# Kernel optimization log

Hardware: AMD Instinct MI355X
Metric: run time of the kernel (lower is better)

## Reference

```python
import jax, jax.numpy as jnp
import numpy as np

B, T, D, H, L = 2, 2048, 2048, 16, 64
HD = D // H  # 128
EPS = 1e-5


def setup_inputs() -> dict:
    key = jax.random.key(0)
    ks = jax.random.split(key, 16)
    s = 0.02
    inp = {
        'x': jax.random.normal(ks[0], (B, T, D), jnp.float32),
        'mask': jnp.tril(jnp.ones((T, T), dtype=bool)),
        'ln_w': jnp.ones((D,), jnp.float32),
        'ln_b': jnp.zeros((D,), jnp.float32),
        'wq': jax.random.normal(ks[1], (D, D), jnp.float32) * s,
        'bq': jnp.zeros((D,), jnp.float32),
        'wk': jax.random.normal(ks[2], (D, D), jnp.float32) * s,
        'bk': jnp.zeros((D,), jnp.float32),
        'wv': jax.random.normal(ks[3], (D, D), jnp.float32) * s,
        'bv': jnp.zeros((D,), jnp.float32),
        'wo': jax.random.normal(ks[4], (D, D), jnp.float32) * s,
        'bo': jnp.zeros((D,), jnp.float32),
        'wcq': jax.random.normal(ks[5], (HD, L), jnp.float32) * s,
        'bcq': jnp.zeros((L,), jnp.float32),
        'wck': jax.random.normal(ks[6], (HD, L), jnp.float32) * s,
        'bck': jnp.zeros((L,), jnp.float32),
        'wcv': jax.random.normal(ks[7], (HD, L), jnp.float32) * s,
        'bcv': jnp.zeros((L,), jnp.float32),
        'wd': jax.random.normal(ks[8], (L, HD), jnp.float32) * s,
        'bd': jnp.zeros((HD,), jnp.float32),
    }
    # standard RoPE frequency table: theta_i = 10000^{-2i/HD}
    inv_freq = 1.0 / (10000.0 ** (jnp.arange(0, HD, 2, dtype=jnp.float32) / HD))
    ang = jnp.arange(T, dtype=jnp.float32)[:, None] * inv_freq[None, :]  # [T, HD/2]
    inp['freqs_cos'] = jnp.cos(ang)
    inp['freqs_sin'] = jnp.sin(ang)
    return inp


def _rope(x, cos, sin):
    # x: [B,T,H,HD]; cos/sin: [T, HD/2]; interleaved (even=real, odd=imag)
    xr, xi = x[..., 0::2], x[..., 1::2]
    c = cos[None, :, None, :]
    sn = sin[None, :, None, :]
    out_r = xr * c - xi * sn
    out_i = xr * sn + xi * c
    return jnp.stack([out_r, out_i], axis=-1).reshape(x.shape)


def reference(x, mask, freqs_cos, freqs_sin, ln_w, ln_b, wq, bq, wk, bk, wv, bv,
              wo, bo, wcq, bcq, wck, bck, wcv, bcv, wd, bd):
    # LayerNorm
    mu = jnp.mean(x, axis=-1, keepdims=True)
    var = jnp.mean(jnp.square(x - mu), axis=-1, keepdims=True)
    xn = (x - mu) / jnp.sqrt(var + EPS) * ln_w + ln_b

    q = (xn @ wq + bq).reshape(B, T, H, HD)
    k = (xn @ wk + bk).reshape(B, T, H, HD)
    v = (xn @ wv + bv).reshape(B, T, H, HD)

    q, k = _rope(q, freqs_cos, freqs_sin), _rope(k, freqs_cos, freqs_sin)

    # compress each head to the latent dim
    q_lat = q @ wcq + bcq  # [B,T,H,L]
    k_lat = k @ wck + bck
    v_lat = v @ wcv + bcv

    scale = 1.0 / np.sqrt(L).astype(np.float32)
    scores = jnp.einsum('bqhl,bkhl->bhqk', q_lat, k_lat) * scale  # [B,H,T,T]
    additive = jnp.where(mask, 0.0, -1e9).astype(scores.dtype)  # bool mask -> additive
    scores = scores + additive[None, None, :, :]
    attn = jax.nn.softmax(scores, axis=-1)

    out = jnp.einsum('bhqk,bkhl->bqhl', attn, v_lat)  # [B,T,H,L]
    out = (out @ wd + bd).reshape(B, T, D)  # decompress to head_dim, merge heads
    return out @ wo + bo
```

## Files before the change

### kernel.cpp

```cpp
#include <hip/hip_runtime.h>
#include <hip/hip_bf16.h>
#include <stdint.h>

#define BB 2
#define TB 2048
#define DB 2048
#define HB 16
#define HDB 128
#define LB 64
#define MB 4096

typedef __hip_bfloat16 bf16;
typedef __attribute__((ext_vector_type(8))) short bf16x8;
typedef __attribute__((ext_vector_type(4))) float f32x4;

#define MFMA_16x16x32 __builtin_amdgcn_mfma_f32_16x16x32_bf16

typedef __attribute__((address_space(3))) void lds_t;
typedef const __attribute__((address_space(1))) void gvm_t;

static __device__ __forceinline__ float bf2f(bf16 h) { return __bfloat162float(h); }
static __device__ __forceinline__ bf16 f2bf(float f) { return __float2bfloat16(f); }
union BV8 { bf16x8 v; bf16 e[8]; };

#define SWZC(r) (((r) ^ ((r) >> 3)) & 7)

__device__ void do_ln(const float* __restrict__ x, const float* __restrict__ g,
                      const float* __restrict__ be, bf16* __restrict__ xn,
                      int row, int tid, char* sm) {
  float* red = (float*)sm;
  const float4* xr = (const float4*)(x + (size_t)row * DB);
  float4 a = xr[2 * tid], b = xr[2 * tid + 1];
  float s = a.x + a.y + a.z + a.w + b.x + b.y + b.z + b.w;
  float s2 = a.x * a.x + a.y * a.y + a.z * a.z + a.w * a.w +
             b.x * b.x + b.y * b.y + b.z * b.z + b.w * b.w;
  for (int off = 32; off > 0; off >>= 1) {
    s += __shfl_down(s, off);
    s2 += __shfl_down(s2, off);
  }
  int w = tid >> 6, lane = tid & 63;
  if (lane == 0) { red[w] = s; red[4 + w] = s2; }
  __syncthreads();
  s = red[0] + red[1] + red[2] + red[3];
  s2 = red[4] + red[5] + red[6] + red[7];
  float mu = s * (1.f / DB);
  float var = s2 * (1.f / DB) - mu * mu;
  float rstd = rsqrtf(var + 1e-5f);
  const float4* gw = (const float4*)g;
  const float4* bb = (const float4*)be;
  float4 g0 = gw[2 * tid], g1 = gw[2 * tid + 1];
  float4 b0 = bb[2 * tid], b1 = bb[2 * tid + 1];
  BV8 u;
  u.e[0] = f2bf((a.x - mu) * rstd * g0.x + b0.x);
  u.e[1] = f2bf((a.y - mu) * rstd * g0.y + b0.y);
  u.e[2] = f2bf((a.z - mu) * rstd * g0.z + b0.z);
  u.e[3] = f2bf((a.w - mu) * rstd * g0.w + b0.w);
  u.e[4] = f2bf((b.x - mu) * rstd * g1.x + b1.x);
  u.e[5] = f2bf((b.y - mu) * rstd * g1.y + b1.y);
  u.e[6] = f2bf((b.z - mu) * rstd * g1.z + b1.z);
  u.e[7] = f2bf((b.w - mu) * rstd * g1.w + b1.w);
  *(bf16x8*)(xn + (size_t)row * DB + tid * 8) = u.v;
}

__device__ void do_wconv(const float* __restrict__ W, bf16* __restrict__ Wt,
                         int bx, int by, int tid, char* sm) {
  float(*t)[33] = (float(*)[33])sm;
  int c0 = bx * 32, r0 = by * 32;
  int tx = tid & 31, ty = tid >> 5;
  for (int p = 0; p < 4; ++p)
    t[ty + 8 * p][tx] = W[(size_t)(r0 + ty + 8 * p) * DB + c0 + tx];
  __syncthreads();
  for (int p = 0; p < 4; ++p)
    Wt[(size_t)(c0 + ty + 8 * p) * DB + r0 + tx] = f2bf(t[tx][ty + 8 * p]);
}

__device__ void do_fold_v(const float* __restrict__ wv, const float* __restrict__ wcv,
                          bf16* __restrict__ BtV, int bx, int h, int tid, char* sm) {
  float(*wvs)[36] = (float(*)[36])sm;
  int k0 = bx * 128;
  int l = tid & 63, ks = tid >> 6;
  float acc[32];
#pragma unroll
  for (int i = 0; i < 32; ++i) acc[i] = 0.f;
  for (int dc = 0; dc < 128; dc += 32) {
    __syncthreads();
    for (int i = tid; i < 128 * 32; i += 256) {
      int kk = i >> 5, dd = i & 31;
      wvs[kk][dd] = wv[(size_t)(k0 + kk) * DB + h * 128 + dc + dd];
    }
    __syncthreads();
    float wr[32];
#pragma unroll
    for (int dd = 0; dd < 32; ++dd) wr[dd] = wcv[(dc + dd) * 64 + l];
#pragma unroll
    for (int i = 0; i < 32; ++i) {
      const float4* row = (const float4*)&wvs[ks * 32 + i][0];
#pragma unroll
      for (int d4 = 0; d4 < 8; ++d4) {
        float4 w4 = row[d4];
        acc[i] += w4.x * wr[d4 * 4] + w4.y * wr[d4 * 4 + 1] +
                  w4.z * wr[d4 * 4 + 2] + w4.w * wr[d4 * 4 + 3];
      }
    }
  }
  bf16* dst = BtV + (size_t)(h * 64 + l) * DB + k0 + ks * 32;
#pragma unroll
  for (int i8 = 0; i8 < 4; ++i8) {
    BV8 u;
#pragma unroll
    for (int j = 0; j < 8; ++j) u.e[j] = f2bf(acc[i8 * 8 + j]);
    *(bf16x8*)(dst + i8 * 8) = u.v;
  }
}

__device__ void do_fold_o(const float* __restrict__ wo, const float* __restrict__ wd,
                          bf16* __restrict__ BtO, int bx, int h, int tid, char* sm) {
  float(*wos)[132] = (float(*)[132])sm;
  int n0 = bx * 128;
  int l = tid & 63, ns = tid >> 6;
  float acc[32];
#pragma unroll
  for (int i = 0; i < 32; ++i) acc[i] = 0.f;
  for (int dc = 0; dc < 128; dc += 32) {
    __syncthreads();
    for (int i = tid; i < 32 * 128; i += 256) {
      int dd = i >> 7, nn = i & 127;
      wos[dd][nn] = wo[(size_t)(h * 128 + dc + dd) * DB + n0 + nn];
    }
    __syncthreads();
    float wr[32];
#pragma unroll
    for (int d4 = 0; d4 < 8; ++d4) {
      float4 w4 = *(const float4*)&wd[l * 128 + dc + d4 * 4];
      wr[d4 * 4] = w4.x; wr[d4 * 4 + 1] = w4.y;
      wr[d4 * 4 + 2] = w4.z; wr[d4 * 4 + 3] = w4.w;
    }
#pragma unroll
    for (int dd = 0; dd < 32; ++dd) {
      float w = wr[dd];
      const float4* row = (const float4*)&wos[dd][ns * 32];
#pragma unroll
      for (int i4 = 0; i4 < 8; ++i4) {
        float4 a4 = row[i4];
        acc[i4 * 4 + 0] += a4.x * w; acc[i4 * 4 + 1] += a4.y * w;
        acc[i4 * 4 + 2] += a4.z * w; acc[i4 * 4 + 3] += a4.w * w;
      }
    }
  }
#pragma unroll
  for (int i = 0; i < 32; ++i)
    BtO[(size_t)(n0 + ns * 32 + i) * 1024 + h * 64 + l] = f2bf(acc[i]);
}

__global__ __launch_bounds__(256) void prep_kernel(
    const float* __restrict__ x, const float* __restrict__ ln_w,
    const float* __restrict__ ln_b, bf16* __restrict__ xn,
    const float* __restrict__ wq, const float* __restrict__ wk,
    bf16* __restrict__ wqkT,
    const float* __restrict__ wv, const float* __restrict__ wcv,
    bf16* __restrict__ BtV,
    const float* __restrict__ wo, const float* __restrict__ wd,
    bf16* __restrict__ BtO,
    const float* __restrict__ bv, const float* __restrict__ bcv,
    float* __restrict__ bvlat,
    const float* __restrict__ bd, const float* __restrict__ bo,
    float* __restrict__ bo2) {
  __shared__ __align__(16) char sm[18432];
  int b = blockIdx.x, tid = threadIdx.x;
  if (b < 4096) {
    do_ln(x, ln_w, ln_b, xn, b, tid, sm);
  } else if (b < 8192) {
    int bb = b - 4096;
    do_wconv(wq, wqkT, bb & 63, bb >> 6, tid, sm);
  } else if (b < 12288) {
    int bb = b - 8192;
    do_wconv(wk, wqkT + (size_t)2048 * 2048, bb & 63, bb >> 6, tid, sm);
  } else if (b < 12544) {
    int bb = b - 12288;
    do_fold_v(wv, wcv, BtV, bb & 15, bb >> 4, tid, sm);
  } else if (b < 12800) {
    int bb = b - 12544;
    do_fold_o(wo, wd, BtO, bb & 15, bb >> 4, tid, sm);
  } else if (b < 12804) {
    int j = (b - 12800) * 256 + tid;
    int h = j >> 6, l = j & 63;
    float s = bcv[l];
    for (int d = 0; d < 128; ++d) s += bv[h * 128 + d] * wcv[d * 64 + l];
    bvlat[j] = s;
  } else {
    float(*red)[64] = (float(*)[64])sm;
    int nl = tid & 63, ks = tid >> 6;
    int n = (b - 12804) * 64 + nl;
    float s = 0.f;
    for (int k = ks * 512; k < ks * 512 + 512; ++k)
      s += bd[k & 127] * wo[(size_t)k * DB + n];
    red[ks][nl] = s;
    __syncthreads();
    if (ks == 0) bo2[n] = bo[n] + red[0][nl] + red[1][nl] + red[2][nl] + red[3][nl];
  }
}

__global__ __launch_bounds__(256) void gemm_qkv_kernel(
    const bf16* __restrict__ A, const bf16* __restrict__ wqkT,
    const bf16* __restrict__ BtV,
    const float* __restrict__ bq, const float* __restrict__ bk,
    const float* __restrict__ bvl,
    const float* __restrict__ wcq, const float* __restrict__ wck,
    const float* __restrict__ bcq, const float* __restrict__ bck,
    bf16* __restrict__ qlat, bf16* __restrict__ klat, bf16* __restrict__ vlatT,
    const float* __restrict__ fcos, const float* __restrict__ fsin) {
  constexpr int K = DB;
  __shared__ __align__(16) char smem[49152];
  bf16* As = (bf16*)smem;
  bf16* Bs = (bf16*)(smem + 8192);
  bf16* Qt = (bf16*)smem;
  bf16* Wt = (bf16*)(smem + 32768);
  int tid = threadIdx.x;
  int m0 = blockIdx.y * 128, n0 = blockIdx.x * 128;
  int w = tid >> 6, l = tid & 63;
  int wr = w >> 1, wc = w & 1;
  int lrow = l & 15, lk = (l >> 4) * 8, ck = l >> 4;
  const bf16* Bsrc = (n0 < 4096) ? (wqkT + (size_t)n0 * K)
                                 : (BtV + (size_t)(n0 - 4096) * K);
  int sel = n0 >> 11;

  if (sel < 2) {
    const float* wcp = sel == 0 ? wcq : wck;
    for (int i = tid; i < 8192; i += 256) {
      int d = i >> 6, j = i & 63;
      Wt[j * 128 + (((d >> 3) ^ (j & 7)) * 8) + (d & 7)] = f2bf(wcp[d * 64 + j]);
    }
  }

  f32x4 zero4 = {0.f, 0.f, 0.f, 0.f};
  f32x4 acc[4][4];
  for (int m = 0; m < 4; ++m)
    for (int n = 0; n < 4; ++n) acc[m][n] = zero4;

  for (int kk = 0; kk < K / 32; ++kk) {
    int k0 = kk * 32;
    __syncthreads();
#pragma unroll
    for (int i = 0; i < 2; ++i) {
      int c = i * 256 + tid;
      int r = c >> 2, cc = c & 3;
      int cb = i * 256 + (tid & ~63);
      __builtin_amdgcn_global_load_lds(
          (gvm_t*)&A[(size_t)(m0 + r) * K + k0 + cc * 8], (lds_t*)&As[cb * 8], 16, 0, 0);
      __builtin_amdgcn_global_load_lds(
          (gvm_t*)&Bsrc[(size_t)r * K + k0 + cc * 8], (lds_t*)&Bs[cb * 8], 16, 0, 0);
    }
    __syncthreads();
    bf16x8 af[4], bfr[4];
    for (int m = 0; m < 4; ++m)
      af[m] = *(bf16x8*)&As[(wr * 64 + m * 16 + lrow) * 32 + lk];
    for (int n = 0; n < 4; ++n)
      bfr[n] = *(bf16x8*)&Bs[(wc * 64 + n * 16 + lrow) * 32 + lk];
    for (int m = 0; m < 4; ++m)
      for (int n = 0; n < 4; ++n)
        acc[m][n] = MFMA_16x16x32(af[m], bfr[n], acc[m][n], 0, 0, 0);
  }

  int rg = 4 * (l >> 4), cl = l & 15;
  if (sel == 2) {
    for (int mf = 0; mf < 4; ++mf) {
      int rowb = m0 + wr * 64 + mf * 16 + rg;
      for (int nf = 0; nf < 4; ++nf) {
        int col = n0 + wc * 64 + nf * 16 + cl;
        int colV = col - 4096;
        float bv_ = bvl[colV];
        size_t vbase = ((size_t)((rowb >> 11) * HB + (colV >> 6)) * 64 + (colV & 63)) * TB
                       + (rowb & (TB - 1));
        for (int r = 0; r < 4; ++r)
          vlatT[vbase + r] = f2bf(acc[mf][nf][r] + bv_);
      }
    }
    return;
  }

  const float* bias = sel == 0 ? bq : bk;
  __syncthreads();
  for (int mf = 0; mf < 4; ++mf) {
    int rowb = m0 + wr * 64 + mf * 16 + rg;
    int rl0 = wr * 64 + mf * 16 + rg;
    for (int nf = 0; nf < 4; ++nf) {
      int col = n0 + wc * 64 + nf * 16 + cl;
      int colL = col & 2047;
      int cloc = wc * 64 + nf * 16 + cl;
      float bv_ = bias[colL];
      for (int r = 0; r < 4; ++r) {
        int rr = rowb + r;
        float v = acc[mf][nf][r] + bv_;
        float pv = __shfl_xor(v, 1);
        int t = rr & (TB - 1);
        int pi = (col & 127) >> 1;
        float c = fcos[t * 64 + pi], sn = fsin[t * 64 + pi];
        v = (col & 1) ? (pv * sn + v * c) : (v * c - pv * sn);
        int rl = rl0 + r;
        Qt[rl * 128 + ((((cloc >> 3) ^ (rl & 7)) * 8) + (cloc & 7))] = f2bf(v);
      }
    }
  }
  __syncthreads();
  f32x4 pacc[2][4];
#pragma unroll
  for (int mi = 0; mi < 2; ++mi)
#pragma unroll
    for (int nf = 0; nf < 4; ++nf) pacc[mi][nf] = zero4;
#pragma unroll
  for (int kc = 0; kc < 4; ++kc) {
    bf16x8 aq[2], bw[4];
#pragma unroll
    for (int mi = 0; mi < 2; ++mi) {
      int row = w * 32 + mi * 16 + lrow;
      aq[mi] = *(bf16x8*)&Qt[row * 128 + (((kc * 4 + ck) ^ (row & 7)) * 8)];
    }
#pragma unroll
    for (int nf = 0; nf < 4; ++nf) {
      int jrow = nf * 16 + lrow;
      bw[nf] = *(bf16x8*)&Wt[jrow * 128 + (((kc * 4 + ck) ^ (jrow & 7)) * 8)];
    }
#pragma unroll
    for (int mi = 0; mi < 2; ++mi)
#pragma unroll
      for (int nf = 0; nf < 4; ++nf)
        pacc[mi][nf] = MFMA_16x16x32(aq[mi], bw[nf], pacc[mi][nf], 0, 0, 0);
  }
  int head = (n0 & 2047) >> 7;
  const float* bias2 = sel == 0 ? bcq : bck;
  bf16* outp = sel == 0 ? qlat : klat;
#pragma unroll
  for (int mi = 0; mi < 2; ++mi)
#pragma unroll
    for (int nf = 0; nf < 4; ++nf) {
      int colj = nf * 16 + cl;
      float b2 = bias2[colj];
#pragma unroll
      for (int r = 0; r < 4; ++r) {
        int roG = m0 + w * 32 + mi * 16 + rg + r;
        outp[((size_t)roG * HB + head) * 64 + colj] = f2bf(pacc[mi][nf][r] + b2);
      }
    }
}

__global__ __launch_bounds__(256) void gemm_out_kernel(
    const bf16* __restrict__ A, const bf16* __restrict__ Bt,
    const float* __restrict__ bias, float* __restrict__ Cout) {
  constexpr int K = 1024, N = DB;
  __shared__ __align__(16) bf16 As[128 * 32];
  __shared__ __align__(16) bf16 Bs[128 * 32];
  int tid = threadIdx.x;
  int m0 = blockIdx.y * 128, n0 = blockIdx.x * 128;
  int w = tid >> 6, l = tid & 63;
  int wr = w >> 1, wc = w & 1;
  int lrow = l & 15, lk = (l >> 4) * 8;

  f32x4 zero4 = {0.f, 0.f, 0.f, 0.f};
  f32x4 acc[4][4];
  for (int m = 0; m < 4; ++m)
    for (int n = 0; n < 4; ++n) acc[m][n] = zero4;

  for (int kk = 0; kk < K / 32; ++kk) {
    int k0 = kk * 32;
    __syncthreads();
#pragma unroll
    for (int i = 0; i < 2; ++i) {
      int c = i * 256 + tid;
      int r = c >> 2, cc = c & 3;
      int cb = i * 256 + (tid & ~63);
      __builtin_amdgcn_global_load_lds(
          (gvm_t*)&A[(size_t)(m0 + r) * K + k0 + cc * 8], (lds_t*)&As[cb * 8], 16, 0, 0);
      __builtin_amdgcn_global_load_lds(
          (gvm_t*)&Bt[(size_t)(n0 + r) * K + k0 + cc * 8], (lds_t*)&Bs[cb * 8], 16, 0, 0);
    }
    __syncthreads();
    bf16x8 af[4], bfr[4];
    for (int m = 0; m < 4; ++m)
      af[m] = *(bf16x8*)&As[(wr * 64 + m * 16 + lrow) * 32 + lk];
    for (int n = 0; n < 4; ++n)
      bfr[n] = *(bf16x8*)&Bs[(wc * 64 + n * 16 + lrow) * 32 + lk];
    for (int m = 0; m < 4; ++m)
      for (int n = 0; n < 4; ++n)
        acc[m][n] = MFMA_16x16x32(af[m], bfr[n], acc[m][n], 0, 0, 0);
  }

  int rg = 4 * (l >> 4), cl = l & 15;
  for (int m = 0; m < 4; ++m) {
    int rowb = m0 + wr * 64 + m * 16 + rg;
    for (int n = 0; n < 4; ++n) {
      int col = n0 + wc * 64 + n * 16 + cl;
      float bv = bias[col];
      for (int r = 0; r < 4; ++r)
        Cout[(size_t)(rowb + r) * N + col] = acc[m][n][r] + bv;
    }
  }
}

__global__ __launch_bounds__(256) void attn_kernel(const bf16* __restrict__ qlat,
                                                   const bf16* __restrict__ klat,
                                                   const bf16* __restrict__ vlatT,
                                                   bf16* __restrict__ aout) {
  int tid = threadIdx.x, w = tid >> 6, l = tid & 63;
  int job = ((int)blockIdx.x & 7) * 64 + ((int)blockIdx.x >> 3);
  int bh = job >> 4, pair = job & 15;
  int h = bh & 15, b = bh >> 4;
  int lrow = l & 15, ck = l >> 4, hi4 = l >> 4;
  __shared__ __align__(16) bf16 Ks[64 * 64];
  __shared__ __align__(16) bf16 VsT[64 * 64];
  __shared__ __align__(16) bf16 Ps[4][16 * 64];
  f32x4 zero4 = {0.f, 0.f, 0.f, 0.f};

  for (int half = 0; half < 2; ++half) {
    int tile = half ? pair : 31 - pair;
    int q0 = tile * 64;
    const bf16* qp = qlat + ((size_t)(b * TB + q0 + w * 16 + lrow) * HB + h) * LB;
    bf16x8 qf0 = *(const bf16x8*)(qp + ck * 8);
    bf16x8 qf1 = *(const bf16x8*)(qp + 32 + ck * 8);
    float mr[4], lsum[4];
    f32x4 o[4];
    for (int r = 0; r < 4; ++r) { mr[r] = -1e30f; lsum[r] = 0.f; }
    for (int n = 0; n < 4; ++n) o[n] = zero4;

    for (int kt = 0; kt <= tile; ++kt) {
      int kv0 = kt * 64;
      __syncthreads();
#pragma unroll
      for (int i = 0; i < 2; ++i) {
        int c = i * 256 + tid;
        int row = c >> 3, ch = c & 7;
        int dst = (c & ~63) * 8;
        __builtin_amdgcn_global_load_lds(
            (gvm_t*)(klat + ((size_t)(b * TB + kv0 + row) * HB + h) * LB + ((ch ^ SWZC(row)) * 8)),
            (lds_t*)&Ks[dst], 16, 0, 0);
        __builtin_amdgcn_global_load_lds(
            (gvm_t*)(vlatT + ((size_t)bh * 64 + row) * TB + kv0 + ((ch ^ SWZC(row)) * 8)),
            (lds_t*)&VsT[dst], 16, 0, 0);
      }
      __syncthreads();
      f32x4 s[4];
      __builtin_amdgcn_s_setprio(1);
#pragma unroll
      for (int kg = 0; kg < 4; ++kg) {
        int row = kg * 16 + lrow;
        int sw = SWZC(row);
        bf16x8 kf0 = *(bf16x8*)&Ks[row * 64 + ((ck ^ sw) * 8)];
        bf16x8 kf1 = *(bf16x8*)&Ks[row * 64 + (((ck + 4) ^ sw) * 8)];
        f32x4 a = zero4;
        a = MFMA_16x16x32(qf0, kf0, a, 0, 0, 0);
        a = MFMA_16x16x32(qf1, kf1, a, 0, 0, 0);
        s[kg] = a;
      }
      __builtin_amdgcn_s_setprio(0);
      float sc[4][4];
      bool diag = (kt == tile);
#pragma unroll
      for (int kg = 0; kg < 4; ++kg)
#pragma unroll
        for (int r = 0; r < 4; ++r) {
          float v = s[kg][r] * 0.125f;
          if (diag) {
            int kvg = kv0 + kg * 16 + lrow;
            int qr = q0 + w * 16 + 4 * hi4 + r;
            if (kvg > qr) v = -1e30f;
          }
          sc[kg][r] = v;
        }
      float rm[4], f[4], psum[4];
#pragma unroll
      for (int r = 0; r < 4; ++r)
        rm[r] = fmaxf(fmaxf(sc[0][r], sc[1][r]), fmaxf(sc[2][r], sc[3][r]));
      for (int off = 8; off > 0; off >>= 1)
#pragma unroll
        for (int r = 0; r < 4; ++r) rm[r] = fmaxf(rm[r], __shfl_xor(rm[r], off));
#pragma unroll
      for (int r = 0; r < 4; ++r) {
        float mn = fmaxf(mr[r], rm[r]);
        f[r] = __expf(mr[r] - mn);
        mr[r] = mn;
      }
#pragma unroll
      for (int kg = 0; kg < 4; ++kg)
#pragma unroll
        for (int r = 0; r < 4; ++r) sc[kg][r] = __expf(sc[kg][r] - mr[r]);
#pragma unroll
      for (int r = 0; r < 4; ++r)
        psum[r] = sc[0][r] + sc[1][r] + sc[2][r] + sc[3][r];
      for (int off = 8; off > 0; off >>= 1)
#pragma unroll
        for (int r = 0; r < 4; ++r) psum[r] += __shfl_xor(psum[r], off);
#pragma unroll
      for (int r = 0; r < 4; ++r) lsum[r] = lsum[r] * f[r] + psum[r];
#pragma unroll
      for (int n = 0; n < 4; ++n) {
        f32x4 t = o[n];
        t[0] *= f[0]; t[1] *= f[1]; t[2] *= f[2]; t[3] *= f[3];
        o[n] = t;
      }
#pragma unroll
      for (int r = 0; r < 4; ++r) {
        int rq = 4 * hi4 + r;
        int sw8 = SWZC(rq) << 3;
#pragma unroll
        for (int kg = 0; kg < 4; ++kg)
          Ps[w][rq * 64 + ((kg * 16 + lrow) ^ sw8)] = f2bf(sc[kg][r]);
      }
      int swp = SWZC(lrow);
      bf16x8 pa0 = *(bf16x8*)&Ps[w][lrow * 64 + ((ck ^ swp) * 8)];
      bf16x8 pa1 = *(bf16x8*)&Ps[w][lrow * 64 + (((ck + 4) ^ swp) * 8)];
      __builtin_amdgcn_s_setprio(1);
#pragma unroll
      for (int n = 0; n < 4; ++n) {
        int row = n * 16 + lrow;
        int sw = SWZC(row);
        bf16x8 vf0 = *(bf16x8*)&VsT[row * 64 + ((ck ^ sw) * 8)];
        bf16x8 vf1 = *(bf16x8*)&VsT[row * 64 + (((ck + 4) ^ sw) * 8)];
        o[n] = MFMA_16x16x32(pa0, vf0, o[n], 0, 0, 0);
        o[n] = MFMA_16x16x32(pa1, vf1, o[n], 0, 0, 0);
      }
      __builtin_amdgcn_s_setprio(0);
    }
    float inv[4];
#pragma unroll
    for (int r = 0; r < 4; ++r) inv[r] = 1.f / lsum[r];
#pragma unroll
    for (int n = 0; n < 4; ++n)
#pragma unroll
      for (int r = 0; r < 4; ++r) {
        size_t row = (size_t)b * TB + q0 + w * 16 + 4 * hi4 + r;
        aout[(row * HB + h) * LB + n * 16 + lrow] = f2bf(o[n][r] * inv[r]);
      }
  }
}

extern "C" void kernel_launch(void* const* d_in, const int* in_sizes, int n_in,
                              void* d_out, int out_size, void* d_ws, size_t ws_size,
                              hipStream_t stream) {
  const float* x    = (const float*)d_in[0];
  const float* ln_w = (const float*)d_in[2];
  const float* ln_b = (const float*)d_in[3];
  const float* wq   = (const float*)d_in[4];
  const float* bq   = (const float*)d_in[5];
  const float* wk   = (const float*)d_in[6];
  const float* bk   = (const float*)d_in[7];
  const float* wv   = (const float*)d_in[8];
  const float* bv   = (const float*)d_in[9];
  const float* wo   = (const float*)d_in[10];
  const float* bo   = (const float*)d_in[11];
  const float* wcq  = (const float*)d_in[12];
  const float* bcq  = (const float*)d_in[13];
  const float* wck  = (const float*)d_in[14];
  const float* bck  = (const float*)d_in[15];
  const float* wcv  = (const float*)d_in[16];
  const float* bcv  = (const float*)d_in[17];
  const float* wd   = (const float*)d_in[18];
  const float* bd   = (const float*)d_in[19];
  const float* fcos = (const float*)d_in[20];
  const float* fsin = (const float*)d_in[21];

  char* ws = (char*)d_ws;
  bf16*  xn    = (bf16*)(ws);
  bf16*  wqkT  = (bf16*)(ws + 16777216);
  bf16*  BtV   = (bf16*)(ws + 33554432);
  bf16*  BtO   = (bf16*)(ws + 37748736);
  bf16*  qlat  = (bf16*)(ws + 41943040);
  bf16*  klat  = (bf16*)(ws + 58720256);
  bf16*  vlatT = (bf16*)(ws + 75497472);
  float* bvlat = (float*)(ws + 83886080);
  float* bo2   = (float*)(ws + 83890176);
  bf16*  aoutp = wqkT;

  prep_kernel<<<12836, 256, 0, stream>>>(
      x, ln_w, ln_b, xn, wq, wk, wqkT, wv, wcv, BtV, wo, wd, BtO,
      bv, bcv, bvlat, bd, bo, bo2);

  gemm_qkv_kernel<<<dim3(40, 32), 256, 0, stream>>>(
      xn, wqkT, BtV, bq, bk, bvlat, wcq, wck, bcq, bck,
      qlat, klat, vlatT, fcos, fsin);

  attn_kernel<<<512, 256, 0, stream>>>(qlat, klat, vlatT, aoutp);

  gemm_out_kernel<<<dim3(16, 32), 256, 0, stream>>>(aoutp, BtO, bo2, (float*)d_out);
}
```

Baseline: 300.8 us.

## Double-buffer K/V tiles in attention and remap GEMM blocks across XCDs

The attention kernel now keeps two LDS buffers for the K and V latent tiles and prefetches the next tile while the current one is computed, so global-to-LDS loads overlap the MFMA and softmax work. It still waits on vmcnt(0) and a barrier at the end of each iteration. Both GEMM kernels switch to a 1-D grid whose block index is remapped so that consecutive tiles land on the same XCD (bid&7 chunking), aiming at better L2 reuse of shared A/B panels. The cost is doubled attention LDS for K/V and a slightly more complex index calculation.

Result: slower. 314.5 us (+4.5%).

```diff
diff --git a/kernel.cpp b/kernel.cpp
--- a/kernel.cpp
+++ b/kernel.cpp
@@ -216,7 +216,10 @@
   bf16* Qt = (bf16*)smem;
   bf16* Wt = (bf16*)(smem + 32768);
   int tid = threadIdx.x;
-  int m0 = blockIdx.y * 128, n0 = blockIdx.x * 128;
+  int bid = blockIdx.x;
+  int j = (bid & 7) * 160 + (bid >> 3);
+  int mt = j / 40, nt = j - mt * 40;
+  int m0 = mt * 128, n0 = nt * 128;
   int w = tid >> 6, l = tid & 63;
   int wr = w >> 1, wc = w & 1;
   int lrow = l & 15, lk = (l >> 4) * 8, ck = l >> 4;
@@ -227,8 +230,8 @@
   if (sel < 2) {
     const float* wcp = sel == 0 ? wcq : wck;
     for (int i = tid; i < 8192; i += 256) {
-      int d = i >> 6, j = i & 63;
-      Wt[j * 128 + (((d >> 3) ^ (j & 7)) * 8) + (d & 7)] = f2bf(wcp[d * 64 + j]);
+      int d = i >> 6, jj = i & 63;
+      Wt[jj * 128 + (((d >> 3) ^ (jj & 7)) * 8) + (d & 7)] = f2bf(wcp[d * 64 + jj]);
     }
   }
 
@@ -350,7 +353,10 @@
   __shared__ __align__(16) bf16 As[128 * 32];
   __shared__ __align__(16) bf16 Bs[128 * 32];
   int tid = threadIdx.x;
-  int m0 = blockIdx.y * 128, n0 = blockIdx.x * 128;
+  int bid = blockIdx.x;
+  int j = (bid & 7) * 64 + (bid >> 3);
+  int mt = j >> 4, nt = j & 15;
+  int m0 = mt * 128, n0 = nt * 128;
   int w = tid >> 6, l = tid & 63;
   int wr = w >> 1, wc = w & 1;
   int lrow = l & 15, lk = (l >> 4) * 8;
@@ -405,10 +411,27 @@
   int bh = job >> 4, pair = job & 15;
   int h = bh & 15, b = bh >> 4;
   int lrow = l & 15, ck = l >> 4, hi4 = l >> 4;
-  __shared__ __align__(16) bf16 Ks[64 * 64];
-  __shared__ __align__(16) bf16 VsT[64 * 64];
+  __shared__ __align__(16) bf16 Ks[2][64 * 64];
+  __shared__ __align__(16) bf16 VsT[2][64 * 64];
   __shared__ __align__(16) bf16 Ps[4][16 * 64];
   f32x4 zero4 = {0.f, 0.f, 0.f, 0.f};
+
+#define ASTAGE(buf, kv0)                                                          \
+  {                                                                               \
+    _Pragma("unroll") for (int i = 0; i < 2; ++i) {                               \
+      int c = i * 256 + tid;                                                      \
+      int row = c >> 3, ch = c & 7;                                               \
+      int dst = (c & ~63) * 8;                                                    \
+      __builtin_amdgcn_global_load_lds(                                           \
+          (gvm_t*)(klat + ((size_t)(b * TB + (kv0) + row) * HB + h) * LB +        \
+                   ((ch ^ SWZC(row)) * 8)),                                       \
+          (lds_t*)&Ks[buf][dst], 16, 0, 0);                                       \
+      __builtin_amdgcn_global_load_lds(                                           \
+          (gvm_t*)(vlatT + ((size_t)bh * 64 + row) * TB + (kv0) +                 \
+                   ((ch ^ SWZC(row)) * 8)),                                       \
+          (lds_t*)&VsT[buf][dst], 16, 0, 0);                                      \
+    }                                                                             \
+  }
 
   for (int half = 0; half < 2; ++half) {
     int tile = half ? pair : 31 - pair;
@@ -421,30 +444,23 @@
     for (int r = 0; r < 4; ++r) { mr[r] = -1e30f; lsum[r] = 0.f; }
     for (int n = 0; n < 4; ++n) o[n] = zero4;
 
+    __syncthreads();
+    ASTAGE(0, 0)
+    asm volatile("s_waitcnt vmcnt(0)");
+    __syncthreads();
+
     for (int kt = 0; kt <= tile; ++kt) {
+      int cur = kt & 1;
       int kv0 = kt * 64;
-      __syncthreads();
-#pragma unroll
-      for (int i = 0; i < 2; ++i) {
-        int c = i * 256 + tid;
-        int row = c >> 3, ch = c & 7;
-        int dst = (c & ~63) * 8;
-        __builtin_amdgcn_global_load_lds(
-            (gvm_t*)(klat + ((size_t)(b * TB + kv0 + row) * HB + h) * LB + ((ch ^ SWZC(row)) * 8)),
-            (lds_t*)&Ks[dst], 16, 0, 0);
-        __builtin_amdgcn_global_load_lds(
-            (gvm_t*)(vlatT + ((size_t)bh * 64 + row) * TB + kv0 + ((ch ^ SWZC(row)) * 8)),
-            (lds_t*)&VsT[dst], 16, 0, 0);
-      }
-      __syncthreads();
+      if (kt < tile) ASTAGE(cur ^ 1, kv0 + 64)
       f32x4 s[4];
       __builtin_amdgcn_s_setprio(1);
 #pragma unroll
       for (int kg = 0; kg < 4; ++kg) {
         int row = kg * 16 + lrow;
         int sw = SWZC(row);
-        bf16x8 kf0 = *(bf16x8*)&Ks[row * 64 + ((ck ^ sw) * 8)];
-        bf16x8 kf1 = *(bf16x8*)&Ks[row * 64 + (((ck + 4) ^ sw) * 8)];
+        bf16x8 kf0 = *(bf16x8*)&Ks[cur][row * 64 + ((ck ^ sw) * 8)];
+        bf16x8 kf1 = *(bf16x8*)&Ks[cur][row * 64 + (((ck + 4) ^ sw) * 8)];
         f32x4 a = zero4;
         a = MFMA_16x16x32(qf0, kf0, a, 0, 0, 0);
         a = MFMA_16x16x32(qf1, kf1, a, 0, 0, 0);
@@ -512,12 +528,14 @@
       for (int n = 0; n < 4; ++n) {
         int row = n * 16 + lrow;
         int sw = SWZC(row);
-        bf16x8 vf0 = *(bf16x8*)&VsT[row * 64 + ((ck ^ sw) * 8)];
-        bf16x8 vf1 = *(bf16x8*)&VsT[row * 64 + (((ck + 4) ^ sw) * 8)];
+        bf16x8 vf0 = *(bf16x8*)&VsT[cur][row * 64 + ((ck ^ sw) * 8)];
+        bf16x8 vf1 = *(bf16x8*)&VsT[cur][row * 64 + (((ck + 4) ^ sw) * 8)];
         o[n] = MFMA_16x16x32(pa0, vf0, o[n], 0, 0, 0);
         o[n] = MFMA_16x16x32(pa1, vf1, o[n], 0, 0, 0);
       }
       __builtin_amdgcn_s_setprio(0);
+      asm volatile("s_waitcnt vmcnt(0)");
+      __syncthreads();
     }
     float inv[4];
 #pragma unroll
@@ -530,6 +548,7 @@
         aout[(row * HB + h) * LB + n * 16 + lrow] = f2bf(o[n][r] * inv[r]);
       }
   }
+#undef ASTAGE
 }
 
 extern "C" void kernel_launch(void* const* d_in, const int* in_sizes, int n_in,
@@ -573,11 +592,11 @@
       x, ln_w, ln_b, xn, wq, wk, wqkT, wv, wcv, BtV, wo, wd, BtO,
       bv, bcv, bvlat, bd, bo, bo2);
 
-  gemm_qkv_kernel<<<dim3(40, 32), 256, 0, stream>>>(
+  gemm_qkv_kernel<<<1280, 256, 0, stream>>>(
       xn, wqkT, BtV, bq, bk, bvlat, wcq, wck, bcq, bck,
       qlat, klat, vlatT, fcos, fsin);
 
   attn_kernel<<<512, 256, 0, stream>>>(qlat, klat, vlatT, aoutp);
 
-  gemm_out_kernel<<<dim3(16, 32), 256, 0, stream>>>(aoutp, BtO, bo2, (float*)d_out);
-}
+  gemm_out_kernel<<<512, 256, 0, stream>>>(aoutp, BtO, bo2, (float*)d_out);
+}
```
